# Kernel tuning notes

Hardware: AMD Instinct MI355X
Metric: run time of the kernel (lower is better)

The kernel has to match this reference:

```python
import jax, jax.numpy as jnp
import numpy as np

EPS = 1e-5  # torch InstanceNorm2d default eps


def instance_norm(x):
    # normalize over spatial dims (H, W) per sample, per channel; affine=False
    mean = jnp.mean(x, axis=(2, 3), keepdims=True)
    var = jnp.var(x, axis=(2, 3), keepdims=True)  # biased var, matching torch
    return (x - mean) * jax.lax.rsqrt(var + EPS)


def conv1x1(x, w, b):
    # x: [B,C,H,W], w: [O,C], b: [O] -> [B,O,H,W]
    return jnp.einsum('oc,bchw->bohw', w, x) + b[None, :, None, None]


def setup_inputs() -> dict:
    key = jax.random.key(0)
    ks = jax.random.split(key, 9)
    B, C, H, W = 4, 64, 96, 96
    fan_out = C  # 1x1 conv: fan_out = out_ch * 1 * 1
    std = float(np.sqrt(2.0 / fan_out))  # kaiming_normal_, mode='fan_out', relu
    x = jax.random.normal(ks[0], (B, C, H, W), dtype=jnp.float32)
    wq = jax.random.normal(ks[1], (C, C), dtype=jnp.float32) * std
    wk = jax.random.normal(ks[2], (C, C), dtype=jnp.float32) * std
    wv = jax.random.normal(ks[3], (C, C), dtype=jnp.float32) * std
    wo = jax.random.normal(ks[4], (C, C), dtype=jnp.float32) * std
    bq = jnp.zeros((C,), dtype=jnp.float32)
    bk = jnp.zeros((C,), dtype=jnp.float32)
    bv = jnp.zeros((C,), dtype=jnp.float32)
    bo = jnp.zeros((C,), dtype=jnp.float32)
    return {"x": x, "wq": wq, "bq": bq, "wk": wk, "bk": bk,
            "wv": wv, "bv": bv, "wo": wo, "bo": bo}


def reference(x, wq, bq, wk, bk, wv, bv, wo, bo):
    B, C, H, W = x.shape
    h = instance_norm(x)
    q = conv1x1(h, wq, bq)  # [B,C,H,W]
    k = conv1x1(h, wk, bk)
    v = conv1x1(h, wv, bv)
    N = H * W
    q = q.reshape(B, C, N).transpose(0, 2, 1)  # [B,N,C]
    k = k.reshape(B, C, N)                     # [B,C,N]
    v = v.reshape(B, C, N).transpose(0, 2, 1)  # [B,N,C]
    scores = jnp.einsum('bnc,bcm->bnm', q, k) * (C ** -0.5)  # [B,N,N]
    attn = jax.nn.softmax(scores, axis=-1)
    o = jnp.einsum('bnm,bmc->bnc', attn, v)  # [B,N,C]
    o = o.reshape(B, H, W, C).transpose(0, 3, 1, 2)  # [B,C,H,W]
    o = conv1x1(o, wo, bo)
    return x + o
```

## Files before the change

### kernel.cpp

```cpp
#include <hip/hip_runtime.h>
#include <stdint.h>

#define BB 4
#define CCH 64
#define NN 9216
#define NTILES 144
#define FTILES 36
#define NCHUNK 5

typedef unsigned short u16;
typedef __attribute__((ext_vector_type(8))) short bhalf8;
typedef __attribute__((ext_vector_type(4))) float f32x4;
typedef __attribute__((ext_vector_type(4))) u16 u16x4;
typedef __attribute__((ext_vector_type(8))) u16 u16x8;
typedef __attribute__((ext_vector_type(2))) unsigned int u32x2;

#define MFMA16(a, b, c) __builtin_amdgcn_mfma_f32_16x16x32_bf16((a), (b), (c), 0, 0, 0)

static __device__ __forceinline__ u16 f2bf(float f) {
  union { float f; unsigned u; } v; v.f = f;
  return (u16)((v.u + 0x7fffu + ((v.u >> 16) & 1u)) >> 16);
}
static __device__ __forceinline__ float bf2f(u16 h) {
  union { unsigned u; float f; } v; v.u = ((unsigned)h) << 16; return v.f;
}
static __device__ __forceinline__ unsigned pk2(float lo, float hi) {
  unsigned a = __float_as_uint(hi) + 0x8000u;
  unsigned b = __float_as_uint(lo) + 0x8000u;
  return __builtin_amdgcn_perm(a, b, 0x07060302u);
}
static __device__ __forceinline__ void glds16(const void* g, void* l) {
  __builtin_amdgcn_global_load_lds(
      (const __attribute__((address_space(1))) unsigned int*)g,
      (__attribute__((address_space(3))) unsigned int*)l, 16, 0, 0);
}

extern "C" __global__ __launch_bounds__(256) void prep_kernel(
    const float* __restrict__ x,
    const float* __restrict__ wq, const float* __restrict__ wk,
    const float* __restrict__ wv, const float* __restrict__ wo,
    float* __restrict__ mean, float* __restrict__ rstd, u16* __restrict__ wbf) {
  if (blockIdx.x >= 256) {
    int i = (blockIdx.x - 256) * 256 + threadIdx.x;
    const float* src = (i < 4096) ? wq : (i < 8192) ? wk : (i < 12288) ? wv : wo;
    wbf[i] = f2bf(src[i & 4095]);
    return;
  }
  int idx = blockIdx.x;
  const f32x4* p4 = (const f32x4*)(x + (size_t)idx * NN);
  float s = 0.f, ss = 0.f;
  for (int i = threadIdx.x; i < NN / 4; i += 256) {
    f32x4 v = p4[i];
#pragma unroll
    for (int j = 0; j < 4; j++) { s += v[j]; ss += v[j] * v[j]; }
  }
#pragma unroll
  for (int o = 32; o > 0; o >>= 1) { s += __shfl_xor(s, o, 64); ss += __shfl_xor(ss, o, 64); }
  __shared__ float ls[4], lss[4];
  int w = threadIdx.x >> 6;
  if ((threadIdx.x & 63) == 0) { ls[w] = s; lss[w] = ss; }
  __syncthreads();
  if (threadIdx.x == 0) {
    s = ls[0] + ls[1] + ls[2] + ls[3];
    ss = lss[0] + lss[1] + lss[2] + lss[3];
    float m = s * (1.f / NN);
    float var = ss * (1.f / NN) - m * m;
    mean[idx] = m;
    rstd[idx] = rsqrtf(var + 1e-5f);
  }
}

extern "C" __global__ __launch_bounds__(256, 4) void qkv_kernel(
    const float* __restrict__ x,
    const float* __restrict__ mean, const float* __restrict__ rstd,
    const u16* __restrict__ wqb, const u16* __restrict__ wkb, const u16* __restrict__ wvb,
    const float* __restrict__ bq, const float* __restrict__ bk,
    u16* __restrict__ Qt, u16* __restrict__ Kt, u16* __restrict__ Vt) {
  __shared__ u16 smem[64 * 72];
  int b = blockIdx.x / NTILES, tile = blockIdx.x % NTILES;
  int n0 = tile * 64;
  int t = threadIdx.x;
  int w = t >> 6, lane = t & 63, q = lane >> 4, ln = lane & 15;
  const float QSCALE = 0.125f * 1.44269504088896340736f;
  const float* mb = mean + b * 64;
  const float* rb_ = rstd + b * 64;
  int nloc = lane;
#pragma unroll
  for (int rep = 0; rep < 4; rep++) {
    int c0 = 16 * w + 4 * rep;
    float h0 = (x[(size_t)(b * 64 + c0 + 0) * NN + n0 + nloc] - mb[c0 + 0]) * rb_[c0 + 0];
    float h1 = (x[(size_t)(b * 64 + c0 + 1) * NN + n0 + nloc] - mb[c0 + 1]) * rb_[c0 + 1];
    float h2 = (x[(size_t)(b * 64 + c0 + 2) * NN + n0 + nloc] - mb[c0 + 2]) * rb_[c0 + 2];
    float h3 = (x[(size_t)(b * 64 + c0 + 3) * NN + n0 + nloc] - mb[c0 + 3]) * rb_[c0 + 3];
    u32x2 hp;
    hp[0] = pk2(h0, h1);
    hp[1] = pk2(h2, h3);
    *(u32x2*)&smem[nloc * 72 + c0] = hp;
  }
  __syncthreads();
  int hrow = (16 * w + ln) * 72;
  bhalf8 hb0 = *(const bhalf8*)&smem[hrow + q * 8];
  bhalf8 hb1 = *(const bhalf8*)&smem[hrow + 32 + q * 8];
  __syncthreads();

  int row_st = t >> 3, ch_st = (t & 7) * 8;
#pragma unroll
  for (int ct = 0; ct < 4; ct++) {
    int wrow = (16 * ct + ln) * 64;
    bhalf8 a0 = *(const bhalf8*)&wqb[wrow + q * 8];
    bhalf8 a1 = *(const bhalf8*)&wqb[wrow + 32 + q * 8];
    f32x4 d = {0.f, 0.f, 0.f, 0.f};
    d = MFMA16(a0, hb0, d);
    d = MFMA16(a1, hb1, d);
    f32x4 b4 = *(const f32x4*)&bq[16 * ct + 4 * q];
    u32x2 pk;
    pk[0] = pk2((d[0] + b4[0]) * QSCALE, (d[1] + b4[1]) * QSCALE);
    pk[1] = pk2((d[2] + b4[2]) * QSCALE, (d[3] + b4[3]) * QSCALE);
    *(u32x2*)&smem[(16 * w + ln) * 68 + 16 * ct + 4 * q] = pk;
  }
  __syncthreads();
#pragma unroll
  for (int pass = 0; pass < 2; pass++) {
    int n = 32 * pass + row_st;
    *(u16x8*)&Qt[(size_t)(b * NN + n0 + n) * 64 + ch_st] = *(const u16x8*)&smem[n * 68 + ch_st];
  }
  __syncthreads();
#pragma unroll
  for (int ct = 0; ct < 4; ct++) {
    int wrow = (16 * ct + ln) * 64;
    bhalf8 a0 = *(const bhalf8*)&wkb[wrow + q * 8];
    bhalf8 a1 = *(const bhalf8*)&wkb[wrow + 32 + q * 8];
    f32x4 d = {0.f, 0.f, 0.f, 0.f};
    d = MFMA16(a0, hb0, d);
    d = MFMA16(a1, hb1, d);
    f32x4 b4 = *(const f32x4*)&bk[16 * ct + 4 * q];
    u32x2 pk;
    pk[0] = pk2(d[0] + b4[0], d[1] + b4[1]);
    pk[1] = pk2(d[2] + b4[2], d[3] + b4[3]);
    *(u32x2*)&smem[(16 * w + ln) * 68 + 16 * ct + 4 * q] = pk;
  }
  __syncthreads();
#pragma unroll
  for (int pass = 0; pass < 2; pass++) {
    int n = 32 * pass + row_st;
    *(u16x8*)&Kt[(size_t)(b * NN + n0 + n) * 64 + ch_st] = *(const u16x8*)&smem[n * 68 + ch_st];
  }
  __syncthreads();
#pragma unroll
  for (int ct = 0; ct < 4; ct++) {
    int wrow = (16 * ct + ln) * 64;
    bhalf8 b0 = *(const bhalf8*)&wvb[wrow + q * 8];
    bhalf8 b1 = *(const bhalf8*)&wvb[wrow + 32 + q * 8];
    f32x4 d = {0.f, 0.f, 0.f, 0.f};
    d = MFMA16(hb0, b0, d);
    d = MFMA16(hb1, b1, d);
    u32x2 pk;
    pk[0] = pk2(d[0], d[1]);
    pk[1] = pk2(d[2], d[3]);
    *(u32x2*)&smem[(16 * ct + ln) * 68 + 16 * w + 4 * q] = pk;
  }
  __syncthreads();
#pragma unroll
  for (int pass = 0; pass < 2; pass++) {
    int c = 32 * pass + row_st;
    *(u16x8*)&Vt[(size_t)(b * 64 + c) * NN + n0 + ch_st] = *(const u16x8*)&smem[c * 68 + ch_st];
  }
}

extern "C" __global__ __launch_bounds__(256, 3) void flash_kernel(
    const u16* __restrict__ Qt, const u16* __restrict__ Kt, const u16* __restrict__ Vt,
    u16* __restrict__ Opart, float* __restrict__ Lsum) {
  __shared__ u16 kbuf[2][64 * 64];
  __shared__ u16 vbuf[2][64 * 64];
  __shared__ u16 pbuf[4][64 * 32];
  int blk = blockIdx.x;
  int b = blk / (FTILES * NCHUNK);
  int rem = blk % (FTILES * NCHUNK);
  int tile = rem / NCHUNK, chunk = rem % NCHUNK;
  int it0 = chunk * 28 + (chunk < 4 ? chunk : 4);
  int nit = 28 + (chunk < 4 ? 1 : 0);
  int m_start = it0 * 64;
  int t = threadIdx.x;
  int w = t >> 6, lane = t & 63, q = lane >> 4, ln = lane & 15;
  int n0w = tile * 256 + 64 * w;
  bhalf8 qf0[4], qf1[4];
#pragma unroll
  for (int s = 0; s < 4; s++) {
    const u16* qp = Qt + (size_t)(b * NN + n0w + 16 * s + ln) * 64 + q * 8;
    qf0[s] = *(const bhalf8*)qp;
    qf1[s] = *(const bhalf8*)(qp + 32);
  }
  const short ONE = 0x3F80;
  const bhalf8 ones = {ONE, ONE, ONE, ONE, ONE, ONE, ONE, ONE};
  f32x4 o[4][4];
  f32x4 lacc[4];
#pragma unroll
  for (int ct = 0; ct < 4; ct++) {
    lacc[ct] = (f32x4){0.f, 0.f, 0.f, 0.f};
#pragma unroll
    for (int s = 0; s < 4; s++) o[ct][s] = (f32x4){0.f, 0.f, 0.f, 0.f};
  }
  u16* pw = pbuf[w];
  int row_s = 16 * w + (lane >> 3);
  int usw = (lane & 7) ^ (row_s & 7);
  const u16* kgp = Kt + ((size_t)b * NN + m_start + row_s) * 64 + usw * 8;
  const u16* vgp = Vt + (size_t)(b * 64 + row_s) * NN + m_start + usw * 8;
  int sbase = (q ^ (ln & 7)) * 8;

  {
    u16* kl = &kbuf[0][w * 1024];
    u16* vl = &vbuf[0][w * 1024];
    glds16(kgp, kl); glds16(kgp + 512, kl + 512);
    glds16(vgp, vl); glds16(vgp + (size_t)8 * NN, vl + 512);
    kgp += 4096; vgp += 64;
  }

  for (int i = 0; i < nit; i++) {
    __syncthreads();
    if (i + 1 < nit) {
      u16* kl = &kbuf[(i + 1) & 1][w * 1024];
      u16* vl = &vbuf[(i + 1) & 1][w * 1024];
      glds16(kgp, kl); glds16(kgp + 512, kl + 512);
      glds16(vgp, vl); glds16(vgp + (size_t)8 * NN, vl + 512);
      kgp += 4096; vgp += 64;
    }
    const u16* kb = kbuf[i & 1];
    const u16* vb = vbuf[i & 1];
#pragma unroll
    for (int p = 0; p < 2; p++) {
#pragma unroll
      for (int lm = 0; lm < 2; lm++) {
        int krow = (16 * (2 * p + lm) + ln) * 64;
        bhalf8 ka0 = *(const bhalf8*)&kb[krow + sbase];
        bhalf8 ka1 = *(const bhalf8*)&kb[krow + (sbase ^ 32)];
        int uw = (((2 * lm + (q >> 1)) ^ ((ln >> 1) & 3)) << 3) + ((q & 1) << 2);
#pragma unroll
        for (int s = 0; s < 4; s++) {
          f32x4 acc = {0.f, 0.f, 0.f, 0.f};
          acc = MFMA16(ka0, qf0[s], acc);
          acc = MFMA16(ka1, qf1[s], acc);
          f32x4 pv;
#pragma unroll
          for (int r = 0; r < 4; r++) pv[r] = __builtin_amdgcn_exp2f(acc[r]);
          u32x2 pk;
          pk[0] = pk2(pv[0], pv[1]);
          pk[1] = pk2(pv[2], pv[3]);
          *(u32x2*)&pw[(16 * s + ln) * 32 + uw] = pk;
        }
      }
      int ur = ((q ^ ((ln >> 1) & 3)) << 3);
      bhalf8 pf[4];
#pragma unroll
      for (int s = 0; s < 4; s++) pf[s] = *(const bhalf8*)&pw[(16 * s + ln) * 32 + ur];
#pragma unroll
      for (int s = 0; s < 4; s++) lacc[s] = MFMA16(ones, pf[s], lacc[s]);
#pragma unroll
      for (int ct = 0; ct < 4; ct++) {
        bhalf8 va = *(const bhalf8*)&vb[(16 * ct + ln) * 64 + (sbase ^ (32 * p))];
#pragma unroll
        for (int s = 0; s < 4; s++) o[ct][s] = MFMA16(va, pf[s], o[ct][s]);
      }
    }
  }
  size_t pbase = (size_t)blk * (256 * 64);
#pragma unroll
  for (int s = 0; s < 4; s++) {
    int row = 64 * w + 16 * s + ln;
#pragma unroll
    for (int ct = 0; ct < 4; ct++) {
      u32x2 pk;
      pk[0] = pk2(o[ct][s][0], o[ct][s][1]);
      pk[1] = pk2(o[ct][s][2], o[ct][s][3]);
      *(u32x2*)&Opart[pbase + (size_t)row * 64 + 16 * ct + 4 * q] = pk;
    }
    if (q == 0) Lsum[(size_t)blk * 256 + row] = lacc[s][0];
  }
}

extern "C" __global__ __launch_bounds__(256, 4) void out_kernel(
    const float* __restrict__ x, const u16* __restrict__ wob, const float* __restrict__ bo,
    const u16* __restrict__ Opart, const float* __restrict__ Lsum, const float* __restrict__ bv,
    float* __restrict__ out) {
  __shared__ float fbuf[64 * 68];
  int b = blockIdx.x / NTILES, tile = blockIdx.x % NTILES;
  int t = threadIdx.x;
  int w = t >> 6, lane = t & 63, q = lane >> 4, ln = lane & 15;
  int n0 = tile * 64;
  int ptile = tile >> 2;
  int prow = (tile & 3) * 64 + 16 * w + ln;
  int p0 = (b * FTILES + ptile) * NCHUNK;
  float L = 0.f;
  float acc0[8], acc1[8];
#pragma unroll
  for (int j = 0; j < 8; j++) { acc0[j] = 0.f; acc1[j] = 0.f; }
#pragma unroll
  for (int ch = 0; ch < NCHUNK; ch++) {
    L += Lsum[(size_t)(p0 + ch) * 256 + prow];
    const u16* op = Opart + ((size_t)(p0 + ch) * 256 + prow) * 64;
    u16x8 d0 = *(const u16x8*)(op + 8 * q);
    u16x8 d1 = *(const u16x8*)(op + 32 + 8 * q);
#pragma unroll
    for (int j = 0; j < 8; j++) { acc0[j] += bf2f(d0[j]); acc1[j] += bf2f(d1[j]); }
  }
  float rl = 1.0f / L;
  union { u16x8 us; bhalf8 bh; } A0, A1;
#pragma unroll
  for (int j = 0; j < 8; j++) {
    A0.us[j] = f2bf(acc0[j] * rl + bv[8 * q + j]);
    A1.us[j] = f2bf(acc1[j] * rl + bv[32 + 8 * q + j]);
  }
  bhalf8 a0 = A0.bh, a1 = A1.bh;
#pragma unroll
  for (int ct = 0; ct < 4; ct++) {
    int wrow = (16 * ct + ln) * 64;
    bhalf8 b0 = *(const bhalf8*)&wob[wrow + q * 8];
    bhalf8 b1 = *(const bhalf8*)&wob[wrow + 32 + q * 8];
    f32x4 d = {0.f, 0.f, 0.f, 0.f};
    d = MFMA16(a0, b0, d);
    d = MFMA16(a1, b1, d);
    *(f32x4*)&fbuf[(16 * ct + ln) * 68 + 16 * w + 4 * q] = d;
  }
  __syncthreads();
#pragma unroll
  for (int pass = 0; pass < 4; pass++) {
    int co = 16 * pass + (t >> 4);
    int chk = t & 15;
    f32x4 v = *(const f32x4*)&fbuf[co * 68 + chk * 4];
    size_t base = (size_t)(b * 64 + co) * NN + n0 + chk * 4;
    f32x4 xv = *(const f32x4*)&x[base];
    float bc = bo[co];
    f32x4 ov;
#pragma unroll
    for (int r = 0; r < 4; r++) ov[r] = xv[r] + bc + v[r];
    *(f32x4*)&out[base] = ov;
  }
}

extern "C" void kernel_launch(void* const* d_in, const int* in_sizes, int n_in,
                              void* d_out, int out_size, void* d_ws, size_t ws_size,
                              hipStream_t stream) {
  (void)in_sizes; (void)n_in; (void)out_size; (void)ws_size;
  const float* x  = (const float*)d_in[0];
  const float* wq = (const float*)d_in[1];
  const float* bq = (const float*)d_in[2];
  const float* wk = (const float*)d_in[3];
  const float* bk = (const float*)d_in[4];
  const float* wv = (const float*)d_in[5];
  const float* bv = (const float*)d_in[6];
  const float* wo = (const float*)d_in[7];
  const float* bo = (const float*)d_in[8];
  float* out = (float*)d_out;
  char* ws = (char*)d_ws;
  float* mean = (float*)ws;
  float* rstd = (float*)(ws + 1024);
  u16* wbf = (u16*)(ws + 2048);
  u16* Qt = (u16*)(ws + 36864);
  u16* Kt = Qt + (size_t)BB * NN * 64;
  u16* Vt = Kt + (size_t)BB * NN * 64;
  u16* Opart = Vt + (size_t)BB * NN * 64;
  float* Lsum = (float*)(Opart + (size_t)BB * FTILES * NCHUNK * 256 * 64);
  const u16* wqb = wbf;
  const u16* wkb = wbf + 4096;
  const u16* wvb = wbf + 8192;
  const u16* wob = wbf + 12288;

  prep_kernel<<<320, 256, 0, stream>>>(x, wq, wk, wv, wo, mean, rstd, wbf);
  qkv_kernel<<<BB * NTILES, 256, 0, stream>>>(x, mean, rstd, wqb, wkb, wvb, bq, bk, Qt, Kt, Vt);
  flash_kernel<<<BB * FTILES * NCHUNK, 256, 0, stream>>>(Qt, Kt, Vt, Opart, Lsum);
  out_kernel<<<BB * NTILES, 256, 0, stream>>>(x, wob, bo, Opart, Lsum, bv, out);
}
```

Before: 202.6 us.

## Fuse split-KV reduction and output projection into flash kernel via last-block counter

Removes the separate out_kernel launch. Each flash block increments an atomic counter per (batch, tile), and the last of the NCHUNK blocks reduces the partial outputs, applies the output projection and residual, and writes the result. Shared memory is merged into one buffer so it can be reused as fbuf. This adds a memset launch, an atomic and fences, plus serialized tail work in the final blocks, which has less parallelism than the old 576-block out_kernel.

Measured after the change: 298.2 us. +47.2%, slower.

```diff
diff --git a/kernel.cpp b/kernel.cpp
--- a/kernel.cpp
+++ b/kernel.cpp
@@ -169,10 +169,15 @@
 
 extern "C" __global__ __launch_bounds__(256, 3) void flash_kernel(
     const u16* __restrict__ Qt, const u16* __restrict__ Kt, const u16* __restrict__ Vt,
-    u16* __restrict__ Opart, float* __restrict__ Lsum) {
-  __shared__ u16 kbuf[2][64 * 64];
-  __shared__ u16 vbuf[2][64 * 64];
-  __shared__ u16 pbuf[4][64 * 32];
+    u16* __restrict__ Opart, float* __restrict__ Lsum, unsigned* __restrict__ cnt,
+    const float* __restrict__ x, const u16* __restrict__ wob,
+    const float* __restrict__ bo, const float* __restrict__ bv,
+    float* __restrict__ out) {
+  __shared__ u16 smem[24576];
+  __shared__ int sflag;
+  u16* kbufs = smem;
+  u16* vbufs = smem + 8192;
+  u16* pbufs = smem + 16384;
   int blk = blockIdx.x;
   int b = blk / (FTILES * NCHUNK);
   int rem = blk % (FTILES * NCHUNK);
@@ -200,7 +205,7 @@
 #pragma unroll
     for (int s = 0; s < 4; s++) o[ct][s] = (f32x4){0.f, 0.f, 0.f, 0.f};
   }
-  u16* pw = pbuf[w];
+  u16* pw = pbufs + w * 2048;
   int row_s = 16 * w + (lane >> 3);
   int usw = (lane & 7) ^ (row_s & 7);
   const u16* kgp = Kt + ((size_t)b * NN + m_start + row_s) * 64 + usw * 8;
@@ -208,8 +213,8 @@
   int sbase = (q ^ (ln & 7)) * 8;
 
   {
-    u16* kl = &kbuf[0][w * 1024];
-    u16* vl = &vbuf[0][w * 1024];
+    u16* kl = kbufs + w * 1024;
+    u16* vl = vbufs + w * 1024;
     glds16(kgp, kl); glds16(kgp + 512, kl + 512);
     glds16(vgp, vl); glds16(vgp + (size_t)8 * NN, vl + 512);
     kgp += 4096; vgp += 64;
@@ -218,14 +223,14 @@
   for (int i = 0; i < nit; i++) {
     __syncthreads();
     if (i + 1 < nit) {
-      u16* kl = &kbuf[(i + 1) & 1][w * 1024];
-      u16* vl = &vbuf[(i + 1) & 1][w * 1024];
+      u16* kl = kbufs + ((i + 1) & 1) * 4096 + w * 1024;
+      u16* vl = vbufs + ((i + 1) & 1) * 4096 + w * 1024;
       glds16(kgp, kl); glds16(kgp + 512, kl + 512);
       glds16(vgp, vl); glds16(vgp + (size_t)8 * NN, vl + 512);
       kgp += 4096; vgp += 64;
     }
-    const u16* kb = kbuf[i & 1];
-    const u16* vb = vbuf[i & 1];
+    const u16* kb = kbufs + (i & 1) * 4096;
+    const u16* vb = vbufs + (i & 1) * 4096;
 #pragma unroll
     for (int p = 0; p < 2; p++) {
 #pragma unroll
@@ -275,64 +280,67 @@
     }
     if (q == 0) Lsum[(size_t)blk * 256 + row] = lacc[s][0];
   }
-}
-
-extern "C" __global__ __launch_bounds__(256, 4) void out_kernel(
-    const float* __restrict__ x, const u16* __restrict__ wob, const float* __restrict__ bo,
-    const u16* __restrict__ Opart, const float* __restrict__ Lsum, const float* __restrict__ bv,
-    float* __restrict__ out) {
-  __shared__ float fbuf[64 * 68];
-  int b = blockIdx.x / NTILES, tile = blockIdx.x % NTILES;
-  int t = threadIdx.x;
-  int w = t >> 6, lane = t & 63, q = lane >> 4, ln = lane & 15;
-  int n0 = tile * 64;
-  int ptile = tile >> 2;
-  int prow = (tile & 3) * 64 + 16 * w + ln;
-  int p0 = (b * FTILES + ptile) * NCHUNK;
-  float L = 0.f;
-  float acc0[8], acc1[8];
-#pragma unroll
-  for (int j = 0; j < 8; j++) { acc0[j] = 0.f; acc1[j] = 0.f; }
-#pragma unroll
-  for (int ch = 0; ch < NCHUNK; ch++) {
-    L += Lsum[(size_t)(p0 + ch) * 256 + prow];
-    const u16* op = Opart + ((size_t)(p0 + ch) * 256 + prow) * 64;
-    u16x8 d0 = *(const u16x8*)(op + 8 * q);
-    u16x8 d1 = *(const u16x8*)(op + 32 + 8 * q);
-#pragma unroll
-    for (int j = 0; j < 8; j++) { acc0[j] += bf2f(d0[j]); acc1[j] += bf2f(d1[j]); }
-  }
-  float rl = 1.0f / L;
-  union { u16x8 us; bhalf8 bh; } A0, A1;
-#pragma unroll
-  for (int j = 0; j < 8; j++) {
-    A0.us[j] = f2bf(acc0[j] * rl + bv[8 * q + j]);
-    A1.us[j] = f2bf(acc1[j] * rl + bv[32 + 8 * q + j]);
-  }
-  bhalf8 a0 = A0.bh, a1 = A1.bh;
-#pragma unroll
-  for (int ct = 0; ct < 4; ct++) {
-    int wrow = (16 * ct + ln) * 64;
-    bhalf8 b0 = *(const bhalf8*)&wob[wrow + q * 8];
-    bhalf8 b1 = *(const bhalf8*)&wob[wrow + 32 + q * 8];
-    f32x4 d = {0.f, 0.f, 0.f, 0.f};
-    d = MFMA16(a0, b0, d);
-    d = MFMA16(a1, b1, d);
-    *(f32x4*)&fbuf[(16 * ct + ln) * 68 + 16 * w + 4 * q] = d;
-  }
-  __syncthreads();
-#pragma unroll
-  for (int pass = 0; pass < 4; pass++) {
-    int co = 16 * pass + (t >> 4);
-    int chk = t & 15;
-    f32x4 v = *(const f32x4*)&fbuf[co * 68 + chk * 4];
-    size_t base = (size_t)(b * 64 + co) * NN + n0 + chk * 4;
-    f32x4 xv = *(const f32x4*)&x[base];
-    float bc = bo[co];
-    f32x4 ov;
-#pragma unroll
-    for (int r = 0; r < 4; r++) ov[r] = xv[r] + bc + v[r];
-    *(f32x4*)&out[base] = ov;
+  __syncthreads();
+  if (t == 0) {
+    __threadfence();
+    unsigned old = atomicAdd(&cnt[b * FTILES + tile], 1u);
+    sflag = (old == NCHUNK - 1);
+  }
+  __syncthreads();
+  if (!sflag) return;
+  __threadfence();
+  float* fbuf = (float*)smem;
+  int p0 = (b * FTILES + tile) * NCHUNK;
+#pragma unroll
+  for (int st = 0; st < 4; st++) {
+    int n0 = tile * 256 + st * 64;
+    int prow = st * 64 + 16 * w + ln;
+    float L = 0.f;
+    float acc0[8], acc1[8];
+#pragma unroll
+    for (int j = 0; j < 8; j++) { acc0[j] = 0.f; acc1[j] = 0.f; }
+#pragma unroll
+    for (int ch = 0; ch < NCHUNK; ch++) {
+      L += Lsum[(size_t)(p0 + ch) * 256 + prow];
+      const u16* op = Opart + ((size_t)(p0 + ch) * 256 + prow) * 64;
+      u16x8 d0 = *(const u16x8*)(op + 8 * q);
+      u16x8 d1 = *(const u16x8*)(op + 32 + 8 * q);
+#pragma unroll
+      for (int j = 0; j < 8; j++) { acc0[j] += bf2f(d0[j]); acc1[j] += bf2f(d1[j]); }
+    }
+    float rl = 1.0f / L;
+    union { u16x8 us; bhalf8 bh; } A0, A1;
+#pragma unroll
+    for (int j = 0; j < 8; j++) {
+      A0.us[j] = f2bf(acc0[j] * rl + bv[8 * q + j]);
+      A1.us[j] = f2bf(acc1[j] * rl + bv[32 + 8 * q + j]);
+    }
+    bhalf8 a0 = A0.bh, a1 = A1.bh;
+#pragma unroll
+    for (int ct = 0; ct < 4; ct++) {
+      int wrow = (16 * ct + ln) * 64;
+      bhalf8 b0 = *(const bhalf8*)&wob[wrow + q * 8];
+      bhalf8 b1 = *(const bhalf8*)&wob[wrow + 32 + q * 8];
+      f32x4 d = {0.f, 0.f, 0.f, 0.f};
+      d = MFMA16(a0, b0, d);
+      d = MFMA16(a1, b1, d);
+      *(f32x4*)&fbuf[(16 * ct + ln) * 68 + 16 * w + 4 * q] = d;
+    }
+    __syncthreads();
+#pragma unroll
+    for (int pass = 0; pass < 4; pass++) {
+      int co = 16 * pass + (t >> 4);
+      int chk = t & 15;
+      f32x4 v = *(const f32x4*)&fbuf[co * 68 + chk * 4];
+      size_t base = (size_t)(b * 64 + co) * NN + n0 + chk * 4;
+      f32x4 xv = *(const f32x4*)&x[base];
+      float bc = bo[co];
+      f32x4 ov;
+#pragma unroll
+      for (int r = 0; r < 4; r++) ov[r] = xv[r] + bc + v[r];
+      *(f32x4*)&out[base] = ov;
+    }
+    __syncthreads();
   }
 }
 
@@ -359,13 +367,15 @@
   u16* Vt = Kt + (size_t)BB * NN * 64;
   u16* Opart = Vt + (size_t)BB * NN * 64;
   float* Lsum = (float*)(Opart + (size_t)BB * FTILES * NCHUNK * 256 * 64);
+  unsigned* cnt = (unsigned*)(Lsum + (size_t)BB * FTILES * NCHUNK * 256);
   const u16* wqb = wbf;
   const u16* wkb = wbf + 4096;
   const u16* wvb = wbf + 8192;
   const u16* wob = wbf + 12288;
 
+  hipMemsetAsync(cnt, 0, BB * FTILES * sizeof(unsigned), stream);
   prep_kernel<<<320, 256, 0, stream>>>(x, wq, wk, wv, wo, mean, rstd, wbf);
   qkv_kernel<<<BB * NTILES, 256, 0, stream>>>(x, mean, rstd, wqb, wkb, wvb, bq, bk, Qt, Kt, Vt);
-  flash_kernel<<<BB * FTILES * NCHUNK, 256, 0, stream>>>(Qt, Kt, Vt, Opart, Lsum);
-  out_kernel<<<BB * NTILES, 256, 0, stream>>>(x, wob, bo, Opart, Lsum, bv, out);
-}
+  flash_kernel<<<BB * FTILES * NCHUNK, 256, 0, stream>>>(Qt, Kt, Vt, Opart, Lsum, cnt,
+                                                         x, wob, bo, bv, out);
+}
```
